# Kernel tuning notes

Hardware: AMD Instinct MI355X
Metric: run time of the kernel (lower is better)

Reference implementation:

```python
import jax, jax.numpy as jnp
import numpy as np

B, T, D_IN = 4, 512, 2048
H, G, HD = 16, 4, 128
CACHE = 3584
S = CACHE + T  # max_seq after cache concat
MAX_POS = 8192
EPS = 1e-6


def _rope_tables():
    inv_freq = 1.0 / (10000.0 ** (np.arange(0, HD, 2, dtype=np.float32) / HD))
    pos = np.arange(MAX_POS, dtype=np.float32)
    freqs = np.outer(pos, inv_freq)                      # [MAX_POS, HD//2]
    emb = np.concatenate([freqs, freqs], axis=-1)        # [MAX_POS, HD]
    return jnp.asarray(np.cos(emb)), jnp.asarray(np.sin(emb))


def setup_inputs() -> dict:
    key = jax.random.key(0)
    ks = jax.random.split(key, 8)
    cos, sin = _rope_tables()
    sc = 1.0 / float(np.sqrt(D_IN))
    x = jax.random.normal(ks[0], (B, T, D_IN), jnp.float32)
    mask = jnp.zeros((B, 1, T, S), bool)  # True = masked out
    position_ids = jnp.broadcast_to(CACHE + jnp.arange(T, dtype=jnp.int32), (B, T))
    cache_k = jax.random.normal(ks[1], (B, G, CACHE, HD), jnp.float32)
    cache_v = jax.random.normal(ks[2], (B, G, CACHE, HD), jnp.float32)
    q_w = jax.random.normal(ks[3], (D_IN, H * HD), jnp.float32) * sc
    k_w = jax.random.normal(ks[4], (D_IN, G * HD), jnp.float32) * sc
    v_w = jax.random.normal(ks[5], (D_IN, G * HD), jnp.float32) * sc
    o_w = jax.random.normal(ks[6], (H * HD, D_IN), jnp.float32) * sc
    qn_w = jnp.ones((HD,), jnp.float32)
    kn_w = jnp.ones((HD,), jnp.float32)
    return dict(x=x, mask=mask, cos=cos, sin=sin, position_ids=position_ids,
                cache_k=cache_k, cache_v=cache_v, q_w=q_w, k_w=k_w, v_w=v_w,
                o_w=o_w, qn_w=qn_w, kn_w=kn_w)


def _rms(z, w):
    return z * jax.lax.rsqrt(jnp.mean(z * z, axis=-1, keepdims=True) + EPS) * w


def _rot_half(z):
    z1, z2 = jnp.split(z, 2, axis=-1)
    return jnp.concatenate([-z2, z1], axis=-1)


def _rope(z, c, s):
    return z * c + _rot_half(z) * s


def reference(x, mask, cos, sin, position_ids, cache_k, cache_v,
              q_w, k_w, v_w, o_w, qn_w, kn_w):
    b, t, _ = x.shape
    # projections + per-head RMSNorm (norm over head_dim, order-independent of transpose)
    q = _rms((x @ q_w).reshape(b, t, H, HD), qn_w).transpose(0, 2, 1, 3)  # [b,H,t,hd]
    k = _rms((x @ k_w).reshape(b, t, G, HD), kn_w).transpose(0, 2, 1, 3)  # [b,G,t,hd]
    v = (x @ v_w).reshape(b, t, G, HD).transpose(0, 2, 1, 3)              # [b,G,t,hd]
    c = cos[position_ids][:, None]  # [b,1,t,hd]
    s = sin[position_ids][:, None]
    q = _rope(q, c, s)
    k = _rope(k, c, s)
    # KV-cache concat (uniform prev length == padded max_seq in the original)
    k_full = jnp.concatenate([cache_k, k], axis=2)  # [b,G,S,hd]
    v_full = jnp.concatenate([cache_v, v], axis=2)
    # GQA attention: group queries over KV heads
    qg = q.reshape(b, G, H // G, t, HD)
    scores = jnp.einsum('bghtd,bgsd->bghts', qg, k_full) * (1.0 / float(np.sqrt(HD)))
    scores = scores + jnp.where(mask[:, :, None], -jnp.inf, 0.0)  # mask [b,1,t,S]->[b,1,1,t,S]
    attn = jax.nn.softmax(scores, axis=-1)
    ctx = jnp.einsum('bghts,bgsd->bghtd', attn, v_full)
    ctx = ctx.reshape(b, H, t, HD).transpose(0, 2, 1, 3).reshape(b, t, H * HD)
    return (ctx @ o_w, k_full, v_full)
```

## Files before the change

kernel.cpp:

```cpp
#include <hip/hip_runtime.h>
#include <stdint.h>

typedef unsigned short u16;
typedef __attribute__((ext_vector_type(4))) float f32x4;
typedef __attribute__((ext_vector_type(16))) float f32x16;
typedef __attribute__((ext_vector_type(8))) short s16x8;
typedef __attribute__((ext_vector_type(2))) unsigned u32x2;

__device__ inline u16 f2b(float f){
    uint32_t u = __builtin_bit_cast(uint32_t, f);
    uint32_t r = (u + 0x7fffu + ((u >> 16) & 1u)) >> 16;
    return (u16)r;
}
__device__ inline float b2f(u16 u){
    uint32_t x = ((uint32_t)u) << 16;
    return __builtin_bit_cast(float, x);
}
__device__ inline u32x2 pswap(unsigned a, unsigned b){
    return __builtin_amdgcn_permlane32_swap(a, b, false, false);
}
__device__ inline unsigned pkbf(float lo, float hi){
    unsigned r;
    asm("v_cvt_pk_bf16_f32 %0, %1, %2" : "=v"(r) : "v"(lo), "v"(hi));
    return r;
}

__global__ void convert_x_k(const float* __restrict__ src, u16* __restrict__ dst, int n4){
    int i = blockIdx.x * blockDim.x + threadIdx.x;
    if (i >= n4) return;
    float4 v = ((const float4*)src)[i];
    ushort4 o; o.x = f2b(v.x); o.y = f2b(v.y); o.z = f2b(v.z); o.w = f2b(v.w);
    ((ushort4*)dst)[i] = o;
}

__global__ void transpose_convert_k(const float* __restrict__ src, u16* __restrict__ dst,
                                    int srcCols, int dstLd, int rowOff){
    __shared__ float ls[64][68];
    int r0 = blockIdx.x * 64;
    int c0 = blockIdx.y * 64;
    int t = threadIdx.x;
    #pragma unroll
    for (int i = 0; i < 4; i++){
        int r = i * 16 + (t >> 4);
        int c = (t & 15) * 4;
        float4 v = *(const float4*)(src + (size_t)(r0 + r) * srcCols + c0 + c);
        *(float4*)&ls[r][c] = v;
    }
    __syncthreads();
    #pragma unroll
    for (int i = 0; i < 2; i++){
        int rr = i * 32 + (t >> 3);
        int cc = (t & 7) * 8;
        union { u16 u[8]; uint4 v; } o;
        #pragma unroll
        for (int j = 0; j < 8; j++) o.u[j] = f2b(ls[cc + j][rr]);
        *(uint4*)(dst + (size_t)(rowOff + c0 + rr) * dstLd + r0 + cc) = o.v;
    }
}

__global__ void copy_cache_k_k(const float* __restrict__ ck, float* __restrict__ kfull,
                               u16* __restrict__ kbf, int n4){
    int i = blockIdx.x * blockDim.x + threadIdx.x;
    if (i >= n4) return;
    const int per_bg = 3584 * 128 / 4;
    int bg = i / per_bg, rem = i - bg * per_bg;
    float4 v = ((const float4*)ck)[i];
    size_t dst4 = (size_t)bg * (4096 * 128 / 4) + rem;
    ((float4*)kfull)[dst4] = v;
    ushort4 o; o.x = f2b(v.x); o.y = f2b(v.y); o.z = f2b(v.z); o.w = f2b(v.w);
    ((ushort4*)kbf)[dst4] = o;
}

__global__ void transpose_cache_v_k(const float* __restrict__ cv, float* __restrict__ vfull,
                                    u16* __restrict__ vT){
    __shared__ float ls[64][68];
    int bg = blockIdx.z;
    int s0 = blockIdx.x * 64;
    int d0 = blockIdx.y * 64;
    int t = threadIdx.x;
    #pragma unroll
    for (int i = 0; i < 4; i++){
        int r = i * 16 + (t >> 4);
        int c = (t & 15) * 4;
        float4 v = *(const float4*)(cv + ((size_t)bg * 3584 + s0 + r) * 128 + d0 + c);
        *(float4*)&ls[r][c] = v;
        *(float4*)(vfull + ((size_t)bg * 4096 + s0 + r) * 128 + d0 + c) = v;
    }
    __syncthreads();
    #pragma unroll
    for (int i = 0; i < 2; i++){
        int rr = i * 32 + (t >> 3);
        int cc = (t & 7) * 8;
        union { u16 u[8]; uint4 v; } o;
        #pragma unroll
        for (int j = 0; j < 8; j++) o.u[j] = f2b(ls[cc + j][rr]);
        *(uint4*)(vT + ((size_t)bg * 128 + d0 + rr) * 4096 + s0 + cc) = o.v;
    }
}

__global__ __launch_bounds__(256) void gemm_bt_k(const u16* __restrict__ A, const u16* __restrict__ Bt,
                                                 float* __restrict__ C, int K, int N){
    __shared__ u16 As[128][72];
    __shared__ u16 Bs[128][72];
    int m0 = blockIdx.y * 128;
    int n0 = blockIdx.x * 128;
    int t = threadIdx.x;
    int wave = t >> 6, lane = t & 63;
    int g16 = lane >> 4, l16 = lane & 15;
    int wr = (wave >> 1) * 64, wc = (wave & 1) * 64;
    f32x4 acc[4][4] = {};
    for (int k0 = 0; k0 < K; k0 += 64){
        #pragma unroll
        for (int i = 0; i < 4; i++){
            int r = i * 32 + (t >> 3);
            int cg = (t & 7) * 8;
            *(uint4*)&As[r][cg] = *(const uint4*)(A + (size_t)(m0 + r) * K + k0 + cg);
            *(uint4*)&Bs[r][cg] = *(const uint4*)(Bt + (size_t)(n0 + r) * K + k0 + cg);
        }
        __syncthreads();
        #pragma unroll
        for (int kc = 0; kc < 2; kc++){
            s16x8 af[4], bfx[4];
            #pragma unroll
            for (int mi = 0; mi < 4; mi++) af[mi]  = *(const s16x8*)&As[wr + mi * 16 + l16][kc * 32 + g16 * 8];
            #pragma unroll
            for (int ni = 0; ni < 4; ni++) bfx[ni] = *(const s16x8*)&Bs[wc + ni * 16 + l16][kc * 32 + g16 * 8];
            #pragma unroll
            for (int mi = 0; mi < 4; mi++)
                #pragma unroll
                for (int ni = 0; ni < 4; ni++)
                    acc[mi][ni] = __builtin_amdgcn_mfma_f32_16x16x32_bf16(af[mi], bfx[ni], acc[mi][ni], 0, 0, 0);
        }
        __syncthreads();
    }
    #pragma unroll
    for (int mi = 0; mi < 4; mi++)
        #pragma unroll
        for (int ni = 0; ni < 4; ni++)
            #pragma unroll
            for (int r = 0; r < 4; r++){
                int row = m0 + wr + mi * 16 + g16 * 4 + r;
                int col = n0 + wc + ni * 16 + l16;
                C[(size_t)row * N + col] = acc[mi][ni][r];
            }
}

__global__ void norm_rope_k(const float* __restrict__ proj, const int* __restrict__ pos_ids,
                            const float* __restrict__ cosT, const float* __restrict__ sinT,
                            const float* __restrict__ qn, const float* __restrict__ kn,
                            u16* __restrict__ qbf, u16* __restrict__ kbf, u16* __restrict__ vT,
                            float* __restrict__ kfull, float* __restrict__ vfull){
    int row = blockIdx.x;
    int b = row >> 9, tt = row & 511;
    int wave = threadIdx.x >> 6, lane = threadIdx.x & 63;
    int pos = pos_ids[row];
    float c0 = cosT[(size_t)pos * 128 + lane];
    float c1 = cosT[(size_t)pos * 128 + 64 + lane];
    float s0 = sinT[(size_t)pos * 128 + lane];
    float s1 = sinT[(size_t)pos * 128 + 64 + lane];
    for (int hh = wave * 6; hh < wave * 6 + 6; hh++){
        const float* z = proj + (size_t)row * 3072 + hh * 128;
        float z0 = z[lane], z1 = z[64 + lane];
        if (hh < 20){
            float ss = z0 * z0 + z1 * z1;
            #pragma unroll
            for (int m = 1; m < 64; m <<= 1) ss += __shfl_xor(ss, m);
            float rn = rsqrtf(ss * (1.0f / 128.0f) + 1e-6f);
            const float* w = (hh < 16) ? qn : kn;
            float zn0 = z0 * rn * w[lane], zn1 = z1 * rn * w[64 + lane];
            float o0 = zn0 * c0 - zn1 * s0;
            float o1 = zn1 * c1 + zn0 * s1;
            if (hh < 16){
                u16* q = qbf + (((size_t)(b * 16 + hh)) * 512 + tt) * 128;
                q[lane] = f2b(o0); q[64 + lane] = f2b(o1);
            } else {
                int g = hh - 16;
                size_t idx = (((size_t)(b * 4 + g)) * 4096 + 3584 + tt) * 128;
                kfull[idx + lane] = o0; kfull[idx + 64 + lane] = o1;
                kbf[idx + lane] = f2b(o0); kbf[idx + 64 + lane] = f2b(o1);
            }
        } else {
            int g = hh - 20;
            size_t idx = (((size_t)(b * 4 + g)) * 4096 + 3584 + tt) * 128;
            vfull[idx + lane] = z0; vfull[idx + 64 + lane] = z1;
            size_t tb = ((size_t)(b * 4 + g)) * 128;
            vT[(tb + lane) * 4096 + 3584 + tt] = f2b(z0);
            vT[(tb + 64 + lane) * 4096 + 3584 + tt] = f2b(z1);
        }
    }
}

__device__ inline void stage_load(uint4* kst, uint4* vst, const u16* kb, const u16* vb, int s0, int t){
    #pragma unroll
    for (int j = 0; j < 4; j++){
        int i = t + 256 * j;
        int kg = i >> 4, cg = i & 15;
        kst[j] = *(const uint4*)(kb + (size_t)(s0 + kg) * 128 + cg * 8);
    }
    #pragma unroll
    for (int j = 0; j < 4; j++){
        int i = t + 256 * j;
        int d = i >> 3, cg = i & 7;
        vst[j] = *(const uint4*)(vb + (size_t)d * 4096 + s0 + cg * 8);
    }
}
__device__ inline void stage_write(uint4* smb, const uint4* kst, const uint4* vst, int t){
    #pragma unroll
    for (int j = 0; j < 4; j++){
        int i = t + 256 * j;
        int kg = i >> 4, cg = i & 15;
        smb[cg * 64 + (kg ^ (4 * (cg & 7)))] = kst[j];
    }
    #pragma unroll
    for (int j = 0; j < 4; j++){
        int i = t + 256 * j;
        int d = i >> 3, cg = i & 7;
        smb[1024 + cg * 128 + d] = vst[j];
    }
}

__global__ __launch_bounds__(256, 2) void attn2_k(const u16* __restrict__ qbf, const u16* __restrict__ kbf,
                                                  const u16* __restrict__ vT, u16* __restrict__ opart,
                                                  float* __restrict__ stats){
    __shared__ uint4 sm[4096];
    int fid = blockIdx.x;
    int swz = (fid & 7) * 64 + (fid >> 3);
    int bg = swz >> 5;  int b = bg >> 2, g = bg & 3;
    int lo5 = swz & 31;
    int hq = g * 4 + (lo5 >> 3);
    int qb = (lo5 >> 1) & 3;
    int sh = lo5 & 1;
    int t = threadIdx.x, w = t >> 6, lane = t & 63;
    int l31 = lane & 31, h = lane >> 5;
    int qw = qb * 128 + w * 32 + l31;
    size_t qoff = (((size_t)(b * 16 + hq)) * 512 + qw) * 128;
    s16x8 qf[8];
    #pragma unroll
    for (int m = 0; m < 8; m++) qf[m] = *(const s16x8*)(qbf + qoff + m * 16 + h * 8);

    const u16* kb = kbf + ((size_t)bg) * 4096 * 128 + (size_t)sh * 2048 * 128;
    const u16* vb = vT  + ((size_t)bg) * 128 * 4096 + (size_t)sh * 2048;

    f32x16 oacc[4] = {};
    float m2 = -1e30f, l = 0.f;
    const float scl2 = 0.08838834764831845f * 1.4426950408889634f;

    uint4 kst[4], vst[4];
    stage_load(kst, vst, kb, vb, 0, t);
    stage_write(sm, kst, vst, t);
    __syncthreads();

    for (int it = 0; it < 32; ++it){
        const uint4* B = sm + (it & 1) * 2048;
        if (it + 1 < 32) stage_load(kst, vst, kb, vb, (it + 1) * 64, t);

        f32x16 st[2] = {};
        #pragma unroll
        for (int kt = 0; kt < 2; kt++)
            #pragma unroll
            for (int m = 0; m < 8; m++){
                int c = 2 * m + h;
                s16x8 kf = *(const s16x8*)&B[c * 64 + ((kt * 32 + l31) ^ (4 * (c & 7)))];
                st[kt] = __builtin_amdgcn_mfma_f32_32x32x16_bf16(kf, qf[m], st[kt], 0, 0, 0);
            }
        float p[2][16];
        float mx = -1e30f;
        #pragma unroll
        for (int kt = 0; kt < 2; kt++)
            #pragma unroll
            for (int r = 0; r < 16; r++){ float v = st[kt][r] * scl2; p[kt][r] = v; mx = fmaxf(mx, v); }
        {   u32x2 rr = pswap(__builtin_bit_cast(unsigned, mx), __builtin_bit_cast(unsigned, mx));
            mx = fmaxf(mx, __builtin_bit_cast(float, h ? rr.x : rr.y)); }
        if (__any(mx > m2 + 8.f)){
            float mn = fmaxf(m2, mx);
            float esc = exp2f(m2 - mn);
            m2 = mn; l *= esc;
            #pragma unroll
            for (int d = 0; d < 4; d++)
                #pragma unroll
                for (int r = 0; r < 16; r++) oacc[d][r] *= esc;
        }
        float ls = 0.f;
        #pragma unroll
        for (int kt = 0; kt < 2; kt++)
            #pragma unroll
            for (int r = 0; r < 16; r++){ float pv = exp2f(p[kt][r] - m2); p[kt][r] = pv; ls += pv; }
        {   u32x2 rr = pswap(__builtin_bit_cast(unsigned, ls), __builtin_bit_cast(unsigned, ls));
            l += ls + __builtin_bit_cast(float, h ? rr.x : rr.y); }
        #pragma unroll
        for (int kc = 0; kc < 4; kc++){
            int tt = kc >> 1, cc = kc & 1;
            unsigned A0 = pkbf(p[tt][8 * cc + 0], p[tt][8 * cc + 1]);
            unsigned A1 = pkbf(p[tt][8 * cc + 2], p[tt][8 * cc + 3]);
            unsigned B0 = pkbf(p[tt][8 * cc + 4], p[tt][8 * cc + 5]);
            unsigned B1 = pkbf(p[tt][8 * cc + 6], p[tt][8 * cc + 7]);
            u32x2 w02 = pswap(A0, B0);
            u32x2 w13 = pswap(A1, B1);
            uint4 bw; bw.x = w02.x; bw.y = w13.x; bw.z = w02.y; bw.w = w13.y;
            s16x8 pb = __builtin_bit_cast(s16x8, bw);
            #pragma unroll
            for (int dt = 0; dt < 4; dt++){
                s16x8 vf = *(const s16x8*)&B[1024 + (2 * kc + h) * 128 + dt * 32 + l31];
                oacc[dt] = __builtin_amdgcn_mfma_f32_32x32x16_bf16(vf, pb, oacc[dt], 0, 0, 0);
            }
        }
        __syncthreads();
        if (it + 1 < 32) stage_write(sm + ((it + 1) & 1) * 2048, kst, vst, t);
        __syncthreads();
    }
    size_t rid = ((size_t)(b * 16 + hq)) * 512 + qw;
    u16* ob = opart + ((size_t)sh * 32768 + rid) * 128;
    #pragma unroll
    for (int dt = 0; dt < 4; dt++)
        #pragma unroll
        for (int rg = 0; rg < 4; rg++){
            ushort4 o4;
            o4.x = f2b(oacc[dt][4 * rg + 0]); o4.y = f2b(oacc[dt][4 * rg + 1]);
            o4.z = f2b(oacc[dt][4 * rg + 2]); o4.w = f2b(oacc[dt][4 * rg + 3]);
            *(ushort4*)(ob + dt * 32 + 8 * rg + 4 * h) = o4;
        }
    if (h == 0){
        float2 s2; s2.x = m2; s2.y = l;
        *(float2*)(stats + ((size_t)sh * 32768 + rid) * 2) = s2;
    }
}

__global__ void merge_k(const u16* __restrict__ opart, const float* __restrict__ stats,
                        u16* __restrict__ ctx){
    int gid = blockIdx.x * 256 + threadIdx.x;
    int rid = gid >> 5, dg = (gid & 31) * 4;
    float m0 = stats[(size_t)rid * 2], l0 = stats[(size_t)rid * 2 + 1];
    float m1 = stats[65536 + (size_t)rid * 2], l1 = stats[65536 + (size_t)rid * 2 + 1];
    float M = fmaxf(m0, m1);
    float w0 = exp2f(m0 - M), w1 = exp2f(m1 - M);
    float inv = 1.f / (l0 * w0 + l1 * w1);
    ushort4 a = *(const ushort4*)(opart + (size_t)rid * 128 + dg);
    ushort4 c4 = *(const ushort4*)(opart + 4194304ll + (size_t)rid * 128 + dg);
    int b = rid >> 13, hq = (rid >> 9) & 15, q = rid & 511;
    u16* dst = ctx + ((size_t)(b * 512 + q)) * 2048 + hq * 128 + dg;
    ushort4 o;
    o.x = f2b((b2f(a.x) * w0 + b2f(c4.x) * w1) * inv);
    o.y = f2b((b2f(a.y) * w0 + b2f(c4.y) * w1) * inv);
    o.z = f2b((b2f(a.z) * w0 + b2f(c4.z) * w1) * inv);
    o.w = f2b((b2f(a.w) * w0 + b2f(c4.w) * w1) * inv);
    *(ushort4*)dst = o;
}

extern "C" void kernel_launch(void* const* d_in, const int* in_sizes, int n_in,
                              void* d_out, int out_size, void* d_ws, size_t ws_size,
                              hipStream_t stream){
    const float* x       = (const float*)d_in[0];
    const float* cosT    = (const float*)d_in[2];
    const float* sinT    = (const float*)d_in[3];
    const int*   pos     = (const int*)  d_in[4];
    const float* cache_k = (const float*)d_in[5];
    const float* cache_v = (const float*)d_in[6];
    const float* q_w     = (const float*)d_in[7];
    const float* k_w     = (const float*)d_in[8];
    const float* v_w     = (const float*)d_in[9];
    const float* o_w     = (const float*)d_in[10];
    const float* qn      = (const float*)d_in[11];
    const float* kn      = (const float*)d_in[12];

    float* out   = (float*)d_out;
    float* kfull = out + 4194304;
    float* vfull = out + 12582912;

    char* ws = (char*)d_ws;
    u16*  x_bf   = (u16*) (ws);
    u16*  wqkv_t = (u16*) (ws + 8388608);
    u16*  wo_t   = (u16*) (ws + 20971520);
    float* proj  = (float*)(ws + 29360128);
    u16*  opart  = (u16*) (ws + 29360128);
    float* stats = (float*)(ws + 46137344);
    u16*  q_bf   = (u16*) (ws + 54525952);
    u16*  k_bf   = (u16*) (ws + 62914560);
    u16*  vT_bf  = (u16*) (ws + 79691776);
    u16*  ctx_bf = (u16*) (ws + 96468992);

    convert_x_k<<<4096, 256, 0, stream>>>(x, x_bf, 1048576);
    transpose_convert_k<<<dim3(32, 32), 256, 0, stream>>>(q_w, wqkv_t, 2048, 2048, 0);
    transpose_convert_k<<<dim3(32,  8), 256, 0, stream>>>(k_w, wqkv_t,  512, 2048, 2048);
    transpose_convert_k<<<dim3(32,  8), 256, 0, stream>>>(v_w, wqkv_t,  512, 2048, 2560);
    transpose_convert_k<<<dim3(32, 32), 256, 0, stream>>>(o_w, wo_t,   2048, 2048, 0);
    copy_cache_k_k<<<7168, 256, 0, stream>>>(cache_k, kfull, k_bf, 1835008);
    transpose_cache_v_k<<<dim3(56, 2, 16), 256, 0, stream>>>(cache_v, vfull, vT_bf);
    gemm_bt_k<<<dim3(24, 16), 256, 0, stream>>>(x_bf, wqkv_t, proj, 2048, 3072);
    norm_rope_k<<<2048, 256, 0, stream>>>(proj, pos, cosT, sinT, qn, kn, q_bf, k_bf, vT_bf, kfull, vfull);
    attn2_k<<<512, 256, 0, stream>>>(q_bf, k_bf, vT_bf, opart, stats);
    merge_k<<<4096, 256, 0, stream>>>(opart, stats, ctx_bf);
    gemm_bt_k<<<dim3(16, 16), 256, 0, stream>>>(ctx_bf, wo_t, out, 2048, 2048);
}
```

Baseline: 486.3 us.

## Split attention KV into four shards, use direct-to-LDS GEMM loads, stage V transpose

Attention now uses 512-thread blocks, each covering 256 queries over a quarter of the KV sequence, with four split-softmax partials combined by merge_k. The LDS swizzles are changed, s_setprio is raised around the MFMA bursts, and the max and sum reductions become trees. The GEMM loads tiles with global_load_lds into unpadded LDS, which may cause bank conflicts on the fragment reads. The new V rows are written contiguously and then transposed by a separate kernel instead of being scattered with 2-byte stores, and the workspace is re-laid out so buffers can alias.

Result: slower. 703.2 us (+44.6%).

```diff
diff --git a/kernel.cpp b/kernel.cpp
--- a/kernel.cpp
+++ b/kernel.cpp
@@ -23,6 +23,10 @@
     unsigned r;
     asm("v_cvt_pk_bf16_f32 %0, %1, %2" : "=v"(r) : "v"(lo), "v"(hi));
     return r;
+}
+__device__ inline void gld16(const u16* g, u16* l){
+    __builtin_amdgcn_global_load_lds((const __attribute__((address_space(1))) unsigned int*)g,
+                                     (__attribute__((address_space(3))) unsigned int*)l, 16, 0, 0);
 }
 
 __global__ void convert_x_k(const float* __restrict__ src, u16* __restrict__ dst, int n4){
@@ -98,10 +102,34 @@
     }
 }
 
+__global__ void transpose_vnew_k(const u16* __restrict__ vnew, u16* __restrict__ vT){
+    __shared__ u16 ls[64][72];
+    int bg = blockIdx.z;
+    int t0 = blockIdx.x * 64;
+    int d0 = blockIdx.y * 64;
+    int t = threadIdx.x;
+    #pragma unroll
+    for (int jj = 0; jj < 2; jj++){
+        int row = jj * 32 + (t >> 3);
+        int c8 = (t & 7) * 8;
+        *(uint4*)&ls[row][c8] = *(const uint4*)(vnew + ((size_t)bg * 512 + t0 + row) * 128 + d0 + c8);
+    }
+    __syncthreads();
+    #pragma unroll
+    for (int jj = 0; jj < 2; jj++){
+        int dd = jj * 32 + (t >> 3);
+        int c8 = (t & 7) * 8;
+        union { u16 u[8]; uint4 v; } o;
+        #pragma unroll
+        for (int j = 0; j < 8; j++) o.u[j] = ls[c8 + j][dd];
+        *(uint4*)(vT + ((size_t)bg * 128 + d0 + dd) * 4096 + 3584 + t0 + c8) = o.v;
+    }
+}
+
 __global__ __launch_bounds__(256) void gemm_bt_k(const u16* __restrict__ A, const u16* __restrict__ Bt,
                                                  float* __restrict__ C, int K, int N){
-    __shared__ u16 As[128][72];
-    __shared__ u16 Bs[128][72];
+    __shared__ u16 As[128 * 64];
+    __shared__ u16 Bs[128 * 64];
     int m0 = blockIdx.y * 128;
     int n0 = blockIdx.x * 128;
     int t = threadIdx.x;
@@ -111,25 +139,27 @@
     f32x4 acc[4][4] = {};
     for (int k0 = 0; k0 < K; k0 += 64){
         #pragma unroll
-        for (int i = 0; i < 4; i++){
-            int r = i * 32 + (t >> 3);
-            int cg = (t & 7) * 8;
-            *(uint4*)&As[r][cg] = *(const uint4*)(A + (size_t)(m0 + r) * K + k0 + cg);
-            *(uint4*)&Bs[r][cg] = *(const uint4*)(Bt + (size_t)(n0 + r) * K + k0 + cg);
+        for (int j = 0; j < 4; j++){
+            int slot = t + 256 * j;
+            int row = slot >> 3, cg = slot & 7;
+            gld16(A  + (size_t)(m0 + row) * K + k0 + cg * 8, &As[slot * 8]);
+            gld16(Bt + (size_t)(n0 + row) * K + k0 + cg * 8, &Bs[slot * 8]);
         }
         __syncthreads();
         #pragma unroll
         for (int kc = 0; kc < 2; kc++){
             s16x8 af[4], bfx[4];
             #pragma unroll
-            for (int mi = 0; mi < 4; mi++) af[mi]  = *(const s16x8*)&As[wr + mi * 16 + l16][kc * 32 + g16 * 8];
-            #pragma unroll
-            for (int ni = 0; ni < 4; ni++) bfx[ni] = *(const s16x8*)&Bs[wc + ni * 16 + l16][kc * 32 + g16 * 8];
+            for (int mi = 0; mi < 4; mi++) af[mi]  = *(const s16x8*)&As[(wr + mi * 16 + l16) * 64 + kc * 32 + g16 * 8];
+            #pragma unroll
+            for (int ni = 0; ni < 4; ni++) bfx[ni] = *(const s16x8*)&Bs[(wc + ni * 16 + l16) * 64 + kc * 32 + g16 * 8];
+            __builtin_amdgcn_s_setprio(1);
             #pragma unroll
             for (int mi = 0; mi < 4; mi++)
                 #pragma unroll
                 for (int ni = 0; ni < 4; ni++)
                     acc[mi][ni] = __builtin_amdgcn_mfma_f32_16x16x32_bf16(af[mi], bfx[ni], acc[mi][ni], 0, 0, 0);
+            __builtin_amdgcn_s_setprio(0);
         }
         __syncthreads();
     }
@@ -148,7 +178,7 @@
 __global__ void norm_rope_k(const float* __restrict__ proj, const int* __restrict__ pos_ids,
                             const float* __restrict__ cosT, const float* __restrict__ sinT,
                             const float* __restrict__ qn, const float* __restrict__ kn,
-                            u16* __restrict__ qbf, u16* __restrict__ kbf, u16* __restrict__ vT,
+                            u16* __restrict__ qbf, u16* __restrict__ kbf, u16* __restrict__ vnew,
                             float* __restrict__ kfull, float* __restrict__ vfull){
     int row = blockIdx.x;
     int b = row >> 9, tt = row & 511;
@@ -183,92 +213,99 @@
             int g = hh - 20;
             size_t idx = (((size_t)(b * 4 + g)) * 4096 + 3584 + tt) * 128;
             vfull[idx + lane] = z0; vfull[idx + 64 + lane] = z1;
-            size_t tb = ((size_t)(b * 4 + g)) * 128;
-            vT[(tb + lane) * 4096 + 3584 + tt] = f2b(z0);
-            vT[(tb + 64 + lane) * 4096 + 3584 + tt] = f2b(z1);
+            size_t vn = (((size_t)(b * 4 + g)) * 512 + tt) * 128;
+            vnew[vn + lane] = f2b(z0); vnew[vn + 64 + lane] = f2b(z1);
         }
     }
 }
 
 __device__ inline void stage_load(uint4* kst, uint4* vst, const u16* kb, const u16* vb, int s0, int t){
     #pragma unroll
-    for (int j = 0; j < 4; j++){
-        int i = t + 256 * j;
+    for (int j = 0; j < 2; j++){
+        int i = t + 512 * j;
         int kg = i >> 4, cg = i & 15;
         kst[j] = *(const uint4*)(kb + (size_t)(s0 + kg) * 128 + cg * 8);
     }
     #pragma unroll
-    for (int j = 0; j < 4; j++){
-        int i = t + 256 * j;
+    for (int j = 0; j < 2; j++){
+        int i = t + 512 * j;
         int d = i >> 3, cg = i & 7;
         vst[j] = *(const uint4*)(vb + (size_t)d * 4096 + s0 + cg * 8);
     }
 }
 __device__ inline void stage_write(uint4* smb, const uint4* kst, const uint4* vst, int t){
     #pragma unroll
-    for (int j = 0; j < 4; j++){
-        int i = t + 256 * j;
+    for (int j = 0; j < 2; j++){
+        int i = t + 512 * j;
         int kg = i >> 4, cg = i & 15;
-        smb[cg * 64 + (kg ^ (4 * (cg & 7)))] = kst[j];
-    }
-    #pragma unroll
-    for (int j = 0; j < 4; j++){
-        int i = t + 256 * j;
+        smb[cg * 64 + (kg ^ (cg & 7))] = kst[j];
+    }
+    #pragma unroll
+    for (int j = 0; j < 2; j++){
+        int i = t + 512 * j;
         int d = i >> 3, cg = i & 7;
-        smb[1024 + cg * 128 + d] = vst[j];
-    }
-}
-
-__global__ __launch_bounds__(256, 2) void attn2_k(const u16* __restrict__ qbf, const u16* __restrict__ kbf,
+        smb[1024 + cg * 128 + (d ^ cg)] = vst[j];
+    }
+}
+
+__global__ __launch_bounds__(512, 4) void attn2_k(const u16* __restrict__ qbf, const u16* __restrict__ kbf,
                                                   const u16* __restrict__ vT, u16* __restrict__ opart,
                                                   float* __restrict__ stats){
     __shared__ uint4 sm[4096];
     int fid = blockIdx.x;
-    int swz = (fid & 7) * 64 + (fid >> 3);
-    int bg = swz >> 5;  int b = bg >> 2, g = bg & 3;
-    int lo5 = swz & 31;
-    int hq = g * 4 + (lo5 >> 3);
-    int qb = (lo5 >> 1) & 3;
-    int sh = lo5 & 1;
+    int bgsh = fid & 63, inner = fid >> 6;
+    int bg = bgsh >> 2, sh = bgsh & 3;
+    int b = bg >> 2, g = bg & 3;
+    int hq = g * 4 + (inner >> 1);
+    int qb = inner & 1;
     int t = threadIdx.x, w = t >> 6, lane = t & 63;
     int l31 = lane & 31, h = lane >> 5;
-    int qw = qb * 128 + w * 32 + l31;
+    int qw = qb * 256 + w * 32 + l31;
     size_t qoff = (((size_t)(b * 16 + hq)) * 512 + qw) * 128;
     s16x8 qf[8];
     #pragma unroll
     for (int m = 0; m < 8; m++) qf[m] = *(const s16x8*)(qbf + qoff + m * 16 + h * 8);
 
-    const u16* kb = kbf + ((size_t)bg) * 4096 * 128 + (size_t)sh * 2048 * 128;
-    const u16* vb = vT  + ((size_t)bg) * 128 * 4096 + (size_t)sh * 2048;
+    const u16* kb = kbf + ((size_t)bg) * 4096 * 128 + (size_t)sh * 1024 * 128;
+    const u16* vb = vT  + ((size_t)bg) * 128 * 4096 + (size_t)sh * 1024;
 
     f32x16 oacc[4] = {};
     float m2 = -1e30f, l = 0.f;
     const float scl2 = 0.08838834764831845f * 1.4426950408889634f;
 
-    uint4 kst[4], vst[4];
+    uint4 kst[2], vst[2];
     stage_load(kst, vst, kb, vb, 0, t);
     stage_write(sm, kst, vst, t);
     __syncthreads();
 
-    for (int it = 0; it < 32; ++it){
+    for (int it = 0; it < 16; ++it){
         const uint4* B = sm + (it & 1) * 2048;
-        if (it + 1 < 32) stage_load(kst, vst, kb, vb, (it + 1) * 64, t);
+        if (it + 1 < 16) stage_load(kst, vst, kb, vb, (it + 1) * 64, t);
 
         f32x16 st[2] = {};
+        __builtin_amdgcn_s_setprio(1);
         #pragma unroll
         for (int kt = 0; kt < 2; kt++)
             #pragma unroll
             for (int m = 0; m < 8; m++){
                 int c = 2 * m + h;
-                s16x8 kf = *(const s16x8*)&B[c * 64 + ((kt * 32 + l31) ^ (4 * (c & 7)))];
+                s16x8 kf = *(const s16x8*)&B[c * 64 + ((kt * 32 + l31) ^ (c & 7))];
                 st[kt] = __builtin_amdgcn_mfma_f32_32x32x16_bf16(kf, qf[m], st[kt], 0, 0, 0);
             }
-        float p[2][16];
-        float mx = -1e30f;
+        __builtin_amdgcn_s_setprio(0);
         #pragma unroll
         for (int kt = 0; kt < 2; kt++)
             #pragma unroll
-            for (int r = 0; r < 16; r++){ float v = st[kt][r] * scl2; p[kt][r] = v; mx = fmaxf(mx, v); }
+            for (int r = 0; r < 16; r++) st[kt][r] *= scl2;
+        float t16[16], t8[8], t4[4], t2[2];
+        #pragma unroll
+        for (int r = 0; r < 16; r++) t16[r] = fmaxf(st[0][r], st[1][r]);
+        #pragma unroll
+        for (int r = 0; r < 8; r++) t8[r] = fmaxf(t16[r], t16[r + 8]);
+        #pragma unroll
+        for (int r = 0; r < 4; r++) t4[r] = fmaxf(t8[r], t8[r + 4]);
+        t2[0] = fmaxf(t4[0], t4[2]); t2[1] = fmaxf(t4[1], t4[3]);
+        float mx = fmaxf(t2[0], t2[1]);
         {   u32x2 rr = pswap(__builtin_bit_cast(unsigned, mx), __builtin_bit_cast(unsigned, mx));
             mx = fmaxf(mx, __builtin_bit_cast(float, h ? rr.x : rr.y)); }
         if (__any(mx > m2 + 8.f)){
@@ -280,36 +317,49 @@
                 #pragma unroll
                 for (int r = 0; r < 16; r++) oacc[d][r] *= esc;
         }
-        float ls = 0.f;
         #pragma unroll
         for (int kt = 0; kt < 2; kt++)
             #pragma unroll
-            for (int r = 0; r < 16; r++){ float pv = exp2f(p[kt][r] - m2); p[kt][r] = pv; ls += pv; }
-        {   u32x2 rr = pswap(__builtin_bit_cast(unsigned, ls), __builtin_bit_cast(unsigned, ls));
-            l += ls + __builtin_bit_cast(float, h ? rr.x : rr.y); }
+            for (int r = 0; r < 16; r++) st[kt][r] = exp2f(st[kt][r] - m2);
+        {
+            float u16a[16], u8[8], u4[4], u2[2];
+            #pragma unroll
+            for (int r = 0; r < 16; r++) u16a[r] = st[0][r] + st[1][r];
+            #pragma unroll
+            for (int r = 0; r < 8; r++) u8[r] = u16a[r] + u16a[r + 8];
+            #pragma unroll
+            for (int r = 0; r < 4; r++) u4[r] = u8[r] + u8[r + 4];
+            u2[0] = u4[0] + u4[2]; u2[1] = u4[1] + u4[3];
+            float ls = u2[0] + u2[1];
+            u32x2 rr = pswap(__builtin_bit_cast(unsigned, ls), __builtin_bit_cast(unsigned, ls));
+            l += ls + __builtin_bit_cast(float, h ? rr.x : rr.y);
+        }
         #pragma unroll
         for (int kc = 0; kc < 4; kc++){
             int tt = kc >> 1, cc = kc & 1;
-            unsigned A0 = pkbf(p[tt][8 * cc + 0], p[tt][8 * cc + 1]);
-            unsigned A1 = pkbf(p[tt][8 * cc + 2], p[tt][8 * cc + 3]);
-            unsigned B0 = pkbf(p[tt][8 * cc + 4], p[tt][8 * cc + 5]);
-            unsigned B1 = pkbf(p[tt][8 * cc + 6], p[tt][8 * cc + 7]);
+            unsigned A0 = pkbf(st[tt][8 * cc + 0], st[tt][8 * cc + 1]);
+            unsigned A1 = pkbf(st[tt][8 * cc + 2], st[tt][8 * cc + 3]);
+            unsigned B0 = pkbf(st[tt][8 * cc + 4], st[tt][8 * cc + 5]);
+            unsigned B1 = pkbf(st[tt][8 * cc + 6], st[tt][8 * cc + 7]);
             u32x2 w02 = pswap(A0, B0);
             u32x2 w13 = pswap(A1, B1);
             uint4 bw; bw.x = w02.x; bw.y = w13.x; bw.z = w02.y; bw.w = w13.y;
             s16x8 pb = __builtin_bit_cast(s16x8, bw);
+            __builtin_amdgcn_s_setprio(1);
             #pragma unroll
             for (int dt = 0; dt < 4; dt++){
-                s16x8 vf = *(const s16x8*)&B[1024 + (2 * kc + h) * 128 + dt * 32 + l31];
+                int c = 2 * kc + h;
+                s16x8 vf = *(const s16x8*)&B[1024 + c * 128 + ((dt * 32 + l31) ^ c)];
                 oacc[dt] = __builtin_amdgcn_mfma_f32_32x32x16_bf16(vf, pb, oacc[dt], 0, 0, 0);
             }
+            __builtin_amdgcn_s_setprio(0);
         }
         __syncthreads();
-        if (it + 1 < 32) stage_write(sm + ((it + 1) & 1) * 2048, kst, vst, t);
+        if (it + 1 < 16) stage_write(sm + ((it + 1) & 1) * 2048, kst, vst, t);
         __syncthreads();
     }
     size_t rid = ((size_t)(b * 16 + hq)) * 512 + qw;
-    u16* ob = opart + ((size_t)sh * 32768 + rid) * 128;
+    u16* ob = opart + ((size_t)sh * 4194304 + rid * 128);
     #pragma unroll
     for (int dt = 0; dt < 4; dt++)
         #pragma unroll
@@ -321,7 +371,7 @@
         }
     if (h == 0){
         float2 s2; s2.x = m2; s2.y = l;
-        *(float2*)(stats + ((size_t)sh * 32768 + rid) * 2) = s2;
+        *(float2*)(stats + (size_t)sh * 65536 + rid * 2) = s2;
     }
 }
 
@@ -329,20 +379,29 @@
                         u16* __restrict__ ctx){
     int gid = blockIdx.x * 256 + threadIdx.x;
     int rid = gid >> 5, dg = (gid & 31) * 4;
-    float m0 = stats[(size_t)rid * 2], l0 = stats[(size_t)rid * 2 + 1];
-    float m1 = stats[65536 + (size_t)rid * 2], l1 = stats[65536 + (size_t)rid * 2 + 1];
-    float M = fmaxf(m0, m1);
-    float w0 = exp2f(m0 - M), w1 = exp2f(m1 - M);
-    float inv = 1.f / (l0 * w0 + l1 * w1);
-    ushort4 a = *(const ushort4*)(opart + (size_t)rid * 128 + dg);
-    ushort4 c4 = *(const ushort4*)(opart + 4194304ll + (size_t)rid * 128 + dg);
+    float ms[4], lsn[4];
+    #pragma unroll
+    for (int s = 0; s < 4; s++){
+        float2 s2 = *(const float2*)(stats + (size_t)s * 65536 + (size_t)rid * 2);
+        ms[s] = s2.x; lsn[s] = s2.y;
+    }
+    float M = fmaxf(fmaxf(ms[0], ms[1]), fmaxf(ms[2], ms[3]));
+    float wsc[4]; float denom = 0.f;
+    #pragma unroll
+    for (int s = 0; s < 4; s++){ wsc[s] = exp2f(ms[s] - M); denom += lsn[s] * wsc[s]; }
+    float inv = 1.f / denom;
+    float acc[4] = {};
+    #pragma unroll
+    for (int s = 0; s < 4; s++){
+        ushort4 a = *(const ushort4*)(opart + (size_t)s * 4194304 + (size_t)rid * 128 + dg);
+        acc[0] += b2f(a.x) * wsc[s]; acc[1] += b2f(a.y) * wsc[s];
+        acc[2] += b2f(a.z) * wsc[s]; acc[3] += b2f(a.w) * wsc[s];
+    }
     int b = rid >> 13, hq = (rid >> 9) & 15, q = rid & 511;
     u16* dst = ctx + ((size_t)(b * 512 + q)) * 2048 + hq * 128 + dg;
     ushort4 o;
-    o.x = f2b((b2f(a.x) * w0 + b2f(c4.x) * w1) * inv);
-    o.y = f2b((b2f(a.y) * w0 + b2f(c4.y) * w1) * inv);
-    o.z = f2b((b2f(a.z) * w0 + b2f(c4.z) * w1) * inv);
-    o.w = f2b((b2f(a.w) * w0 + b2f(c4.w) * w1) * inv);
+    o.x = f2b(acc[0] * inv); o.y = f2b(acc[1] * inv);
+    o.z = f2b(acc[2] * inv); o.w = f2b(acc[3] * inv);
     *(ushort4*)dst = o;
 }
 
@@ -367,12 +426,13 @@
     float* vfull = out + 12582912;
 
     char* ws = (char*)d_ws;
-    u16*  x_bf   = (u16*) (ws);
-    u16*  wqkv_t = (u16*) (ws + 8388608);
-    u16*  wo_t   = (u16*) (ws + 20971520);
-    float* proj  = (float*)(ws + 29360128);
-    u16*  opart  = (u16*) (ws + 29360128);
-    float* stats = (float*)(ws + 46137344);
+    float* proj  = (float*)(ws);
+    u16*  x_bf   = (u16*) (ws + 25165824);
+    u16*  vnew   = (u16*) (ws + 25165824);
+    u16*  opart  = (u16*) (ws);
+    u16*  wqkv_t = (u16*) (ws + 33554432);
+    float* stats = (float*)(ws + 33554432);
+    u16*  wo_t   = (u16*) (ws + 46137344);
     u16*  q_bf   = (u16*) (ws + 54525952);
     u16*  k_bf   = (u16*) (ws + 62914560);
     u16*  vT_bf  = (u16*) (ws + 79691776);
@@ -386,8 +446,9 @@
     copy_cache_k_k<<<7168, 256, 0, stream>>>(cache_k, kfull, k_bf, 1835008);
     transpose_cache_v_k<<<dim3(56, 2, 16), 256, 0, stream>>>(cache_v, vfull, vT_bf);
     gemm_bt_k<<<dim3(24, 16), 256, 0, stream>>>(x_bf, wqkv_t, proj, 2048, 3072);
-    norm_rope_k<<<2048, 256, 0, stream>>>(proj, pos, cosT, sinT, qn, kn, q_bf, k_bf, vT_bf, kfull, vfull);
-    attn2_k<<<512, 256, 0, stream>>>(q_bf, k_bf, vT_bf, opart, stats);
+    norm_rope_k<<<2048, 256, 0, stream>>>(proj, pos, cosT, sinT, qn, kn, q_bf, k_bf, vnew, kfull, vfull);
+    transpose_vnew_k<<<dim3(8, 2, 16), 256, 0, stream>>>(vnew, vT_bf);
+    attn2_k<<<512, 512, 0, stream>>>(q_bf, k_bf, vT_bf, opart, stats);
     merge_k<<<4096, 256, 0, stream>>>(opart, stats, ctx_bf);
     gemm_bt_k<<<dim3(16, 16), 256, 0, stream>>>(ctx_bf, wo_t, out, 2048, 2048);
 }
```
